# Kernel optimization log

Hardware: AMD Instinct MI355X
Metric: run time of the kernel (lower is better)

Reference implementation:

```python
import jax, jax.numpy as jnp
import numpy as np

GROUPS = 4
RATIO = 2


def setup_inputs() -> dict:
    key = jax.random.key(0)
    k1, k2, k3 = jax.random.split(key, 3)
    B, C, H, W = 16, 256, 64, 64
    c_out = 2 * GROUPS * RATIO ** 2  # 32
    x = jax.random.normal(k1, (B, C, H, W), dtype=jnp.float32)
    # offset conv: normal_init std=0.001 (full 1x1 conv)
    w_off = jax.random.normal(k2, (c_out, C), dtype=jnp.float32) * 0.001
    b_off = jnp.zeros((c_out,), dtype=jnp.float32)
    # scope conv: grouped 1x1 (groups=4); init is zeros in the module, use tiny
    # random values so sigmoid != exactly 0.5 and the path is exercised
    w_scope = jax.random.normal(k3, (GROUPS, c_out // GROUPS, C // GROUPS), dtype=jnp.float32) * 0.001
    b_scope = jnp.zeros((c_out,), dtype=jnp.float32)
    return {"x": x, "w_off": w_off, "b_off": b_off, "w_scope": w_scope, "b_scope": b_scope}


def _pixel_shuffle(t, r):
    B, C, H, W = t.shape
    Co = C // (r * r)
    t = t.reshape(B, Co, r, r, H, W)
    t = t.transpose(0, 1, 4, 2, 5, 3)  # B, Co, H, r, W, r
    return t.reshape(B, Co, H * r, W * r)


def _bilinear_border(img, ix, iy):
    # img: (c, H, W); ix, iy: (Ho, Wo) pixel coords in input space
    c, H, W = img.shape
    ix = jnp.clip(ix, 0.0, W - 1.0)  # border padding: clamp coordinate
    iy = jnp.clip(iy, 0.0, H - 1.0)
    x0f = jnp.floor(ix)
    y0f = jnp.floor(iy)
    wx = ix - x0f
    wy = iy - y0f
    x0 = jnp.clip(x0f.astype(jnp.int32), 0, W - 1)
    x1 = jnp.clip(x0 + 1, 0, W - 1)
    y0 = jnp.clip(y0f.astype(jnp.int32), 0, H - 1)
    y1 = jnp.clip(y0 + 1, 0, H - 1)
    v00 = img[:, y0, x0]
    v01 = img[:, y0, x1]
    v10 = img[:, y1, x0]
    v11 = img[:, y1, x1]
    return (v00 * (1 - wy) * (1 - wx) + v01 * (1 - wy) * wx
            + v10 * wy * (1 - wx) + v11 * wy * wx)


def reference(x, w_off, b_off, w_scope, b_scope):
    B, C, H, W = x.shape
    g, r = GROUPS, RATIO
    # offset 1x1 conv
    off = jnp.einsum('bihw,oi->bohw', x, w_off) + b_off[None, :, None, None]
    # grouped scope 1x1 conv + sigmoid scaling
    xgc = x.reshape(B, g, C // g, H, W)
    sc = jnp.einsum('bgihw,goi->bgohw', xgc, w_scope).reshape(B, -1, H, W)
    sc = sc + b_scope[None, :, None, None]
    off = jax.nn.sigmoid(sc) * 0.5 * off
    # pixel shuffle to (B, 2*g, Ho, Wo)
    off = _pixel_shuffle(off, r)
    Ho, Wo = H * r, W * r
    # rearrange: x 'b (c grp) h w -> (b grp) c h w'; offset 'b (grp two) h w -> (b grp) h w two'
    cg = C // g
    xg = x.reshape(B, cg, g, H, W).transpose(0, 2, 1, 3, 4).reshape(B * g, cg, H, W)
    og = off.reshape(B, g, 2, Ho, Wo).transpose(0, 1, 3, 4, 2).reshape(B * g, Ho, Wo, 2)
    # sampling grid: centers + offset, normalized by (Wo, Ho), align_corners=False
    posx = jnp.linspace(0.5, Wo - 0.5, Wo, dtype=x.dtype)[None, :]   # (1, Wo)
    posy = jnp.linspace(0.5, Ho - 0.5, Ho, dtype=x.dtype)[:, None]   # (Ho, 1)
    gx = 2.0 * (posx + og[..., 0]) / Wo - 1.0  # (B*g, Ho, Wo)
    gy = 2.0 * (posy + og[..., 1]) / Ho - 1.0
    # unnormalize (align_corners=False): pix = ((g+1)*size - 1) / 2
    ix = ((gx + 1.0) * W - 1.0) * 0.5
    iy = ((gy + 1.0) * H - 1.0) * 0.5
    out = jax.vmap(_bilinear_border)(xg, ix, iy)  # (B*g, cg, Ho, Wo)
    # rearrange back: '(b grp) c h w -> b (c grp) h w'
    out = out.reshape(B, g, cg, Ho, Wo).transpose(0, 2, 1, 3, 4).reshape(B, C, Ho, Wo)
    return out
```

## Files before the change

### kernel.cpp

```cpp
#include <hip/hip_runtime.h>
#include <math.h>

#define B_   16
#define C_   256
#define H_   64
#define W_   64
#define G_   4
#define HO_  128
#define WO_  128
#define HW_  (H_ * W_)
#define HOWO_ (HO_ * WO_)

__global__ __launch_bounds__(256) void prep_kernel(
    const float* __restrict__ w_off,
    const float* __restrict__ w_scope,
    float* __restrict__ wcomb)
{
    const int k = blockIdx.x * 256 + threadIdx.x;
    if (k >= 8 * 32 * 40) return;
    const int q  = k % 40;
    const int r  = k / 40;
    const int i2 = r & 31;
    const int u  = r >> 5;
    const int v  = u & 3;
    const int hi = u >> 2;
    const int i  = 64 * v + 32 * hi + i2;
    float val;
    if (q < 32) val = w_off[q * 256 + i];
    else        val = w_scope[v * 512 + (q - 32) * 64 + 32 * hi + i2];
    wcomb[k] = val;
}

__global__ __launch_bounds__(512, 6) void fused_kernel(
    const float* __restrict__ x,
    const float* __restrict__ wcomb,
    const float* __restrict__ b_off,
    const float* __restrict__ b_scope,
    float* __restrict__ out)
{
    __shared__ float4 red[8][8][64];
    __shared__ float4 aux[8][64];

    const int tid = threadIdx.x;
    const int u   = __builtin_amdgcn_readfirstlane(tid >> 6);
    const int w   = tid & 63;
    const int v   = u & 3;
    const int hi  = u >> 2;
    const int h   = blockIdx.x & 63;
    const int b   = blockIdx.x >> 6;

    const float* xq = x + (size_t)b * C_ * HW_ +
                      (size_t)(64 * v + 32 * hi) * HW_ + h * W_ + w;
    const float* wt = wcomb + u * (32 * 40);

    float offp[32];
    float scp[8];
#pragma unroll
    for (int j = 0; j < 32; ++j) offp[j] = 0.f;
#pragma unroll
    for (int j = 0; j < 8; ++j) scp[j] = 0.f;

#pragma unroll 4
    for (int i2 = 0; i2 < 32; ++i2) {
        const float xv = xq[(size_t)i2 * HW_];
        const float* wr = wt + i2 * 40;
#pragma unroll
        for (int j = 0; j < 32; ++j) offp[j] += xv * wr[j];
#pragma unroll
        for (int j = 0; j < 8; ++j)  scp[j] += xv * wr[32 + j];
    }

    if (hi) {
#pragma unroll
        for (int j = 0; j < 8; ++j)
            red[4 + v][j][w] = make_float4(offp[4 * j + 0], offp[4 * j + 1],
                                           offp[4 * j + 2], offp[4 * j + 3]);
        aux[2 * v + 0][w] = make_float4(scp[0], scp[1], scp[2], scp[3]);
        aux[2 * v + 1][w] = make_float4(scp[4], scp[5], scp[6], scp[7]);
    }
    __syncthreads();
    if (!hi) {
#pragma unroll
        for (int j = 0; j < 8; ++j) {
            const float4 p = red[4 + v][j][w];
            offp[4 * j + 0] += p.x; offp[4 * j + 1] += p.y;
            offp[4 * j + 2] += p.z; offp[4 * j + 3] += p.w;
        }
        const float4 s0 = aux[2 * v + 0][w];
        const float4 s1 = aux[2 * v + 1][w];
        scp[0] += s0.x; scp[1] += s0.y; scp[2] += s0.z; scp[3] += s0.w;
        scp[4] += s1.x; scp[5] += s1.y; scp[6] += s1.z; scp[7] += s1.w;
#pragma unroll
        for (int j = 0; j < 8; ++j)
            red[v][j][w] = make_float4(offp[4 * j + 0], offp[4 * j + 1],
                                       offp[4 * j + 2], offp[4 * j + 3]);
    }
    __syncthreads();
    if (!hi) {
        float4 a = make_float4(0.f, 0.f, 0.f, 0.f);
        float4 c = make_float4(0.f, 0.f, 0.f, 0.f);
#pragma unroll
        for (int tt = 0; tt < 4; ++tt) {
            const float4 pa = red[tt][2 * v + 0][w];
            const float4 pc = red[tt][2 * v + 1][w];
            a.x += pa.x; a.y += pa.y; a.z += pa.z; a.w += pa.w;
            c.x += pc.x; c.y += pc.y; c.z += pc.z; c.w += pc.w;
        }
        const float ao[8] = {a.x, a.y, a.z, a.w, c.x, c.y, c.z, c.w};
        float f[8];
#pragma unroll
        for (int j = 0; j < 8; ++j) {
            const float offv = ao[j] + b_off[8 * v + j];
            const float scv  = scp[j] + b_scope[8 * v + j];
            f[j] = offv * 0.5f / (1.f + expf(-scv));
        }
#pragma unroll
        for (int r1 = 0; r1 < 2; ++r1) {
            const float hoF = (float)(2 * h + r1);
            float ix0 = ((float)(2 * w + 0) - 0.5f + f[2 * r1 + 0]) * 0.5f;
            float iy0 = (hoF - 0.5f + f[4 + 2 * r1 + 0]) * 0.5f;
            float ix1 = ((float)(2 * w + 1) - 0.5f + f[2 * r1 + 1]) * 0.5f;
            float iy1 = (hoF - 0.5f + f[4 + 2 * r1 + 1]) * 0.5f;
            ix0 = fminf(fmaxf(ix0, 0.f), (float)(W_ - 1));
            iy0 = fminf(fmaxf(iy0, 0.f), (float)(H_ - 1));
            ix1 = fminf(fmaxf(ix1, 0.f), (float)(W_ - 1));
            iy1 = fminf(fmaxf(iy1, 0.f), (float)(H_ - 1));
            aux[2 * v + r1][w] = make_float4(ix0, iy0, ix1, iy1);
        }
    }
    __syncthreads();

    const int wo = tid & 127;
    const int q  = tid >> 7;
    const int z  = q & 1;
    const int gh = q >> 1;
    const int ho = 2 * h + z;

    const float2* cbase = (const float2*)&aux[0][0];
    const float* xb0 = x + (size_t)b * C_ * HW_;
    float* ob0 = out + (size_t)b * C_ * HOWO_ + ho * WO_ + wo;

#pragma unroll
    for (int gg = 0; gg < 2; ++gg) {
        const int g = 2 * gh + gg;
        const float2 c = cbase[(g * 2 + z) * 128 + wo];
        const float ix = c.x, iy = c.y;

        const float x0f = floorf(ix);
        const float y0f = floorf(iy);
        const float wx = ix - x0f;
        const float wy = iy - y0f;
        int x0 = (int)x0f;
        int y0 = (int)y0f;
        x0 = max(0, min(x0, W_ - 1));
        y0 = max(0, min(y0, H_ - 1));
        const int x1 = min(x0 + 1, W_ - 1);
        const int y1 = min(y0 + 1, H_ - 1);

        const float w00 = (1.f - wy) * (1.f - wx);
        const float w01 = (1.f - wy) * wx;
        const float w10 = wy * (1.f - wx);
        const float w11 = wy * wx;

        const int p00 = y0 * W_ + x0;
        const int p01 = y0 * W_ + x1;
        const int p10 = y1 * W_ + x0;
        const int p11 = y1 * W_ + x1;

        const float* xb = xb0 + (size_t)g * HW_;
        float* ob = ob0 + (size_t)g * HOWO_;

#pragma unroll 4
        for (int cc = 0; cc < 64; ++cc) {
            const float* pl = xb + (size_t)cc * 4 * HW_;
            const float val = pl[p00] * w00 + pl[p01] * w01 +
                              pl[p10] * w10 + pl[p11] * w11;
            ob[(size_t)cc * 4 * HOWO_] = val;
        }
    }
}

extern "C" void kernel_launch(void* const* d_in, const int* in_sizes, int n_in,
                              void* d_out, int out_size, void* d_ws, size_t ws_size,
                              hipStream_t stream) {
    const float* x       = (const float*)d_in[0];
    const float* w_off   = (const float*)d_in[1];
    const float* b_off   = (const float*)d_in[2];
    const float* w_scope = (const float*)d_in[3];
    const float* b_scope = (const float*)d_in[4];
    float* out = (float*)d_out;
    float* wcomb = (float*)d_ws;

    prep_kernel<<<dim3(40), 256, 0, stream>>>(w_off, w_scope, wcomb);
    fused_kernel<<<dim3(B_ * H_), 512, 0, stream>>>(
        x, wcomb, b_off, b_scope, out);
}
```

Measured before the change: 93.66 us.

## Split fused conv+sample kernel into separate conv and sampling kernels via workspace coords

Splits the fused kernel into a conv kernel that writes clamped sampling coordinates to a workspace buffer, and a separate sample kernel launched over (ho-pairs, group, batch). The conv kernel now preloads all 32 x values up front and fully unrolls the reduction loop, and the sample kernel uses nontemporal stores for the large output. This decouples the register-heavy conv phase from the bandwidth-bound gather/store phase so each can run at its own occupancy. The cost is an extra launch plus a write and re-read of the coordinate buffer.

Measured after the change: 111.5 us. +19.1%, slower.

```diff
diff --git a/kernel.cpp b/kernel.cpp
--- a/kernel.cpp
+++ b/kernel.cpp
@@ -31,12 +31,12 @@
     wcomb[k] = val;
 }
 
-__global__ __launch_bounds__(512, 6) void fused_kernel(
+__global__ __launch_bounds__(512) void conv_kernel(
     const float* __restrict__ x,
     const float* __restrict__ wcomb,
     const float* __restrict__ b_off,
     const float* __restrict__ b_scope,
-    float* __restrict__ out)
+    float2* __restrict__ coords)
 {
     __shared__ float4 red[8][8][64];
     __shared__ float4 aux[8][64];
@@ -53,6 +53,10 @@
                       (size_t)(64 * v + 32 * hi) * HW_ + h * W_ + w;
     const float* wt = wcomb + u * (32 * 40);
 
+    float xv[32];
+#pragma unroll
+    for (int i2 = 0; i2 < 32; ++i2) xv[i2] = xq[(size_t)i2 * HW_];
+
     float offp[32];
     float scp[8];
 #pragma unroll
@@ -60,14 +64,13 @@
 #pragma unroll
     for (int j = 0; j < 8; ++j) scp[j] = 0.f;
 
-#pragma unroll 4
+#pragma unroll
     for (int i2 = 0; i2 < 32; ++i2) {
-        const float xv = xq[(size_t)i2 * HW_];
         const float* wr = wt + i2 * 40;
 #pragma unroll
-        for (int j = 0; j < 32; ++j) offp[j] += xv * wr[j];
-#pragma unroll
-        for (int j = 0; j < 8; ++j)  scp[j] += xv * wr[32 + j];
+        for (int j = 0; j < 32; ++j) offp[j] += xv[i2] * wr[j];
+#pragma unroll
+        for (int j = 0; j < 8; ++j)  scp[j] += xv[i2] * wr[32 + j];
     }
 
     if (hi) {
@@ -125,58 +128,57 @@
             iy0 = fminf(fmaxf(iy0, 0.f), (float)(H_ - 1));
             ix1 = fminf(fmaxf(ix1, 0.f), (float)(W_ - 1));
             iy1 = fminf(fmaxf(iy1, 0.f), (float)(H_ - 1));
-            aux[2 * v + r1][w] = make_float4(ix0, iy0, ix1, iy1);
-        }
-    }
-    __syncthreads();
-
-    const int wo = tid & 127;
-    const int q  = tid >> 7;
-    const int z  = q & 1;
-    const int gh = q >> 1;
-    const int ho = 2 * h + z;
-
-    const float2* cbase = (const float2*)&aux[0][0];
-    const float* xb0 = x + (size_t)b * C_ * HW_;
-    float* ob0 = out + (size_t)b * C_ * HOWO_ + ho * WO_ + wo;
-
-#pragma unroll
-    for (int gg = 0; gg < 2; ++gg) {
-        const int g = 2 * gh + gg;
-        const float2 c = cbase[(g * 2 + z) * 128 + wo];
-        const float ix = c.x, iy = c.y;
-
-        const float x0f = floorf(ix);
-        const float y0f = floorf(iy);
-        const float wx = ix - x0f;
-        const float wy = iy - y0f;
-        int x0 = (int)x0f;
-        int y0 = (int)y0f;
-        x0 = max(0, min(x0, W_ - 1));
-        y0 = max(0, min(y0, H_ - 1));
-        const int x1 = min(x0 + 1, W_ - 1);
-        const int y1 = min(y0 + 1, H_ - 1);
-
-        const float w00 = (1.f - wy) * (1.f - wx);
-        const float w01 = (1.f - wy) * wx;
-        const float w10 = wy * (1.f - wx);
-        const float w11 = wy * wx;
-
-        const int p00 = y0 * W_ + x0;
-        const int p01 = y0 * W_ + x1;
-        const int p10 = y1 * W_ + x0;
-        const int p11 = y1 * W_ + x1;
-
-        const float* xb = xb0 + (size_t)g * HW_;
-        float* ob = ob0 + (size_t)g * HOWO_;
+            float4* cw = (float4*)&coords[(((size_t)b * G_ + v) * HO_ +
+                                           (2 * h + r1)) * WO_ + 2 * w];
+            *cw = make_float4(ix0, iy0, ix1, iy1);
+        }
+    }
+}
+
+__global__ __launch_bounds__(256) void sample_kernel(
+    const float* __restrict__ x,
+    const float2* __restrict__ coords,
+    float* __restrict__ out)
+{
+    const int wo = threadIdx.x & 127;
+    const int ho = (blockIdx.x << 1) + (threadIdx.x >> 7);
+    const int g  = blockIdx.y;
+    const int b  = blockIdx.z;
+
+    const float2 c = coords[(((size_t)b * G_ + g) * HO_ + ho) * WO_ + wo];
+    const float ix = c.x, iy = c.y;
+
+    const float x0f = floorf(ix);
+    const float y0f = floorf(iy);
+    const float wx = ix - x0f;
+    const float wy = iy - y0f;
+    int x0 = (int)x0f;
+    int y0 = (int)y0f;
+    x0 = max(0, min(x0, W_ - 1));
+    y0 = max(0, min(y0, H_ - 1));
+    const int x1 = min(x0 + 1, W_ - 1);
+    const int y1 = min(y0 + 1, H_ - 1);
+
+    const float w00 = (1.f - wy) * (1.f - wx);
+    const float w01 = (1.f - wy) * wx;
+    const float w10 = wy * (1.f - wx);
+    const float w11 = wy * wx;
+
+    const int p00 = y0 * W_ + x0;
+    const int p01 = y0 * W_ + x1;
+    const int p10 = y1 * W_ + x0;
+    const int p11 = y1 * W_ + x1;
+
+    const float* xb = x + (size_t)b * C_ * HW_ + (size_t)g * HW_;
+    float* ob = out + (size_t)b * C_ * HOWO_ + (size_t)g * HOWO_ +
+                ho * WO_ + wo;
 
 #pragma unroll 4
-        for (int cc = 0; cc < 64; ++cc) {
-            const float* pl = xb + (size_t)cc * 4 * HW_;
-            const float val = pl[p00] * w00 + pl[p01] * w01 +
-                              pl[p10] * w10 + pl[p11] * w11;
-            ob[(size_t)cc * 4 * HOWO_] = val;
-        }
+    for (int cc = 0; cc < 64; ++cc) {
+        const float* pl = xb + (size_t)cc * 4 * HW_;
+        const float v = pl[p00] * w00 + pl[p01] * w01 +
+                        pl[p10] * w10 + pl[p11] * w11;
+        __builtin_nontemporal_store(v, &ob[(size_t)cc * 4 * HOWO_]);
     }
 }
 
@@ -189,9 +191,12 @@
     const float* w_scope = (const float*)d_in[3];
     const float* b_scope = (const float*)d_in[4];
     float* out = (float*)d_out;
+
     float* wcomb = (float*)d_ws;
+    float2* coords = (float2*)((char*)d_ws + 65536);
 
     prep_kernel<<<dim3(40), 256, 0, stream>>>(w_off, w_scope, wcomb);
-    fused_kernel<<<dim3(B_ * H_), 512, 0, stream>>>(
-        x, wcomb, b_off, b_scope, out);
-}
+    conv_kernel<<<dim3(B_ * H_), 512, 0, stream>>>(
+        x, wcomb, b_off, b_scope, coords);
+    sample_kernel<<<dim3(HO_ / 2, G_, B_), 256, 0, stream>>>(x, coords, out);
+}
```
